# Performance work log

Hardware: AMD Instinct MI355X
Metric: run time of the kernel (lower is better)

Reference implementation:

```python
import jax, jax.numpy as jnp
import numpy as np

B, S, D = 4, 2048, 1024
H, DK, DV = 16, 64, 64
SCALE = 8.0  # scaling_factor = sqrt(dk)


def setup_inputs() -> dict:
    key = jax.random.key(0)
    ks = jax.random.split(key, 9)
    s = 1.0 / np.sqrt(D)
    return {
        "q": jax.random.normal(ks[0], (B, S, D), jnp.float32),
        "k": jax.random.normal(ks[1], (B, S, D), jnp.float32),
        "v": jax.random.normal(ks[2], (B, S, D), jnp.float32),
        "Wq": jax.random.uniform(ks[3], (D, H * DK), jnp.float32, -s, s),
        "bq": jax.random.uniform(ks[4], (H * DK,), jnp.float32, -s, s),
        "Wk": jax.random.uniform(ks[5], (D, H * DK), jnp.float32, -s, s),
        "bk": jax.random.uniform(ks[6], (H * DK,), jnp.float32, -s, s),
        "Wv": jax.random.uniform(ks[7], (D, H * DV), jnp.float32, -s, s),
        "bv": jax.random.uniform(ks[8], (H * DV,), jnp.float32, -s, s),
    }


def reference(q, k, v, Wq, bq, Wk, bk, Wv, bv):
    # Linear projections, then split heads: [B,S,H*d] -> [B,S,H,d]
    qh = (q @ Wq + bq).reshape(B, S, H, DK)
    kh = (k @ Wk + bk).reshape(B, S, H, DK)
    vh = (v @ Wv + bv).reshape(B, S, H, DV)
    # scores: [B,H,Sq,Sk]
    e = jnp.einsum("bqhd,bkhd->bhqk", qh, kh) / SCALE
    attn = jax.nn.softmax(e, axis=-1)
    out = jnp.einsum("bhqk,bkhd->bqhd", attn, vh)  # [B,Sq,H,DV]
    return out.reshape(B, S, H * DV)  # dropout p=0 -> identity
```

## Files before the change

### kernel.cpp

```cpp
#include <hip/hip_runtime.h>
#include <hip/hip_bf16.h>


typedef unsigned short u16;
typedef unsigned int   u32;
typedef short bf16x8 __attribute__((ext_vector_type(8)));
typedef short bf16x4 __attribute__((ext_vector_type(4)));
typedef float f32x4  __attribute__((ext_vector_type(4)));
typedef u32   u32x4  __attribute__((ext_vector_type(4)));

#define S_TOT 2048
#define HD    1024
#define QK_SCALE 0.18033688f

#if __has_builtin(__builtin_amdgcn_exp2f)
#define EXP2(x) __builtin_amdgcn_exp2f(x)
#else
#define EXP2(x) exp2f(x)
#endif

__device__ __forceinline__ u16 f2bf(float f) {
  union { float f; unsigned u; } v; v.f = f;
  unsigned r = v.u + 0x7FFFu + ((v.u >> 16) & 1u);
  return (u16)(r >> 16);
}

__device__ __forceinline__ u32 cvt_pk_bf16(float lo, float hi) {
  u32 r;
  asm("v_cvt_pk_bf16_f32 %0, %1, %2" : "=v"(r) : "v"(lo), "v"(hi));
  return r;
}

__device__ __forceinline__ bf16x4 ds_tr16(unsigned a) {
  bf16x4 d;
  asm volatile("ds_read_b64_tr_b16 %0, %1" : "=v"(d) : "v"(a) : "memory");
  return d;
}

__device__ __forceinline__ void gld16(const u16* g, u16* l) {
  __builtin_amdgcn_global_load_lds(
      (const __attribute__((address_space(1))) u32*)g,
      (__attribute__((address_space(3))) u32*)l, 16, 0, 0);
}

#define LGKM_FENCE() do { asm volatile("s_waitcnt lgkmcnt(0)" ::: "memory"); \
                          __builtin_amdgcn_sched_barrier(0); } while (0)

__global__ __launch_bounds__(256)
void conv_kernel(const float* __restrict__ x0, const float* __restrict__ x1, const float* __restrict__ x2,
                 const float* __restrict__ w0, const float* __restrict__ w1, const float* __restrict__ w2,
                 u16* __restrict__ Xb, u16* __restrict__ Wt)
{
  const int z = blockIdx.y;
  const int t = threadIdx.x;
  if (blockIdx.x < 1024) {
    const float* X = z == 0 ? x0 : (z == 1 ? x1 : x2);
    u16* Xz = Xb + (size_t)z * 8388608;
    int tid = blockIdx.x * 256 + t;
#pragma unroll
    for (int i = 0; i < 8; ++i) {
      int c = tid + i * 262144;
      int row = c >> 8, k4 = (c & 255) * 4;
      const float4 xv = *(const float4*)&X[(size_t)row * 1024 + k4];
      int p = (k4 & ~31) + 8 * ((k4 & 15) >> 2) + 4 * ((k4 >> 4) & 1);
      bf16x4 sv = { (short)f2bf(xv.x), (short)f2bf(xv.y), (short)f2bf(xv.z), (short)f2bf(xv.w) };
      *(bf16x4*)&Xz[(size_t)row * 1024 + p] = sv;
    }
  } else {
    const float* W = z == 0 ? w0 : (z == 1 ? w1 : w2);
    u16* Wz = Wt + (size_t)z * 1048576;
    int tid = (blockIdx.x - 1024) * 256 + t;
#pragma unroll
    for (int i = 0; i < 8; ++i) {
      int c = tid + i * 32768;
      int k = c >> 8, n4 = (c & 255) * 4;
      const float4 wv = *(const float4*)&W[(size_t)k * 1024 + n4];
      int off = ((n4 >> 7) * 32 + (k >> 5)) * 4096 + ((n4 >> 4) & 7) * 512
              + ((k >> 4) & 1) * 256 + (k & 15) * 16 + (n4 & 15);
      bf16x4 sv = { (short)f2bf(wv.x), (short)f2bf(wv.y), (short)f2bf(wv.z), (short)f2bf(wv.w) };
      *(bf16x4*)&Wz[off] = sv;
    }
  }
}

__global__ __launch_bounds__(256)
void gemm_kernel(const u16* __restrict__ Xb, const u16* __restrict__ Wt,
                 const float* __restrict__ b0, const float* __restrict__ b1, const float* __restrict__ b2,
                 u16* __restrict__ o0, u16* __restrict__ o1, u16* __restrict__ o2)
{
  int p  = blockIdx.x + 8 * blockIdx.y + 512 * blockIdx.z;
  int wk = (p & 7) * 192 + (p >> 3);
  int nb = wk & 7, mb = (wk >> 3) & 63, z = wk >> 9;

  const u16* Xz = Xb + (size_t)z * 8388608;
  const u16* Wz = Wt + (size_t)z * 1048576;
  const float* BS = z == 0 ? b0 : (z == 1 ? b1 : b2);
  u16*         O  = z == 0 ? o0 : (z == 1 ? o1 : o2);
  const float  osc = (z == 0) ? QK_SCALE : 1.0f;

  const int t = threadIdx.x;
  const int lane = t & 63, wid = t >> 6;
  const int g = lane >> 4, ln = lane & 15;
  const int wm = wid >> 1, wn = wid & 1;
  const int mbase = mb * 128, nbase = nb * 128;

  __shared__ __align__(16) u16 Al[128 * 32];
  __shared__ __align__(16) u16 Bl[16 * 256];

  f32x4 acc[4][4];
#pragma unroll
  for (int i = 0; i < 4; ++i)
#pragma unroll
    for (int j = 0; j < 4; ++j) { acc[i][j][0]=0.f; acc[i][j][1]=0.f; acc[i][j][2]=0.f; acc[i][j][3]=0.f; }

  const u16* sa = Xz + (size_t)(mbase + (t >> 2)) * 1024 + (t & 3) * 8;
  const u16* sb = Wz + (size_t)(nb * 32) * 4096 + t * 8;
  u16* al_w = &Al[wid * 512];
  u16* bl_w = &Bl[wid * 512];

  const unsigned bs_base = (unsigned)(size_t)&Bl[0] + (unsigned)((wn * 4) * 1024) + lane * 8;

  for (int kb = 0; kb < 32; ++kb) {
    gld16(sa + kb * 32,                 al_w);
    gld16(sa + kb * 32 + 64 * 1024,     al_w + 2048);
    gld16(sb + kb * 4096,               bl_w);
    gld16(sb + kb * 4096 + 2048,        bl_w + 2048);
    __syncthreads();

    bf16x8 af[4];
#pragma unroll
    for (int mf = 0; mf < 4; ++mf)
      af[mf] = *(const bf16x8*)&Al[(wm * 64 + mf * 16 + ln) * 32 + g * 8];

    bf16x8 bfv[4];
#pragma unroll
    for (int nf = 0; nf < 4; ++nf) {
      bf16x4 lo = ds_tr16(bs_base + (unsigned)(nf * 1024));
      bf16x4 hi = ds_tr16(bs_base + (unsigned)(nf * 1024 + 512));
      bf16x8 bb;
      bb[0]=lo[0]; bb[1]=lo[1]; bb[2]=lo[2]; bb[3]=lo[3];
      bb[4]=hi[0]; bb[5]=hi[1]; bb[6]=hi[2]; bb[7]=hi[3];
      bfv[nf] = bb;
    }
    LGKM_FENCE();
#pragma unroll
    for (int mf = 0; mf < 4; ++mf)
#pragma unroll
      for (int nf = 0; nf < 4; ++nf)
        acc[mf][nf] = __builtin_amdgcn_mfma_f32_16x16x32_bf16(af[mf], bfv[nf], acc[mf][nf], 0, 0, 0);
    __syncthreads();
  }

#pragma unroll
  for (int nf = 0; nf < 4; ++nf) {
    int n = nbase + wn * 64 + nf * 16 + ln;
    float bv = BS[n];
#pragma unroll
    for (int mf = 0; mf < 4; ++mf)
#pragma unroll
      for (int r = 0; r < 4; ++r) {
        int m = mbase + wm * 64 + mf * 16 + 4 * g + r;
        O[(size_t)m * 1024 + n] = f2bf((acc[mf][nf][r] + bv) * osc);
      }
  }
}

__global__ __launch_bounds__(256)
void proj_kernel(const float* __restrict__ x0, const float* __restrict__ x1, const float* __restrict__ x2,
                 const float* __restrict__ w0, const float* __restrict__ w1, const float* __restrict__ w2,
                 const float* __restrict__ b0, const float* __restrict__ b1, const float* __restrict__ b2,
                 u16* __restrict__ o0, u16* __restrict__ o1, u16* __restrict__ o2)
{
  int p  = blockIdx.x + 8 * blockIdx.y + 512 * blockIdx.z;
  int wk = (p & 7) * 192 + (p >> 3);
  int nb = wk & 7, mb = (wk >> 3) & 63, z = wk >> 9;

  const float* X  = z == 0 ? x0 : (z == 1 ? x1 : x2);
  const float* W  = z == 0 ? w0 : (z == 1 ? w1 : w2);
  const float* BS = z == 0 ? b0 : (z == 1 ? b1 : b2);
  u16*         O  = z == 0 ? o0 : (z == 1 ? o1 : o2);
  const float  osc = (z == 0) ? QK_SCALE : 1.0f;

  const int t = threadIdx.x;
  const int lane = t & 63, wid = t >> 6;
  const int g = lane >> 4, ln = lane & 15;
  const int wm = wid >> 1, wn = wid & 1;
  const int mbase = mb * 128, nbase = nb * 128;

  __shared__ __align__(16) u16 As[128 * 40];
  __shared__ __align__(16) u16 Bs[16 * 272];

  f32x4 acc[4][4];
#pragma unroll
  for (int i = 0; i < 4; ++i)
#pragma unroll
    for (int j = 0; j < 4; ++j) { acc[i][j][0]=0.f; acc[i][j][1]=0.f; acc[i][j][2]=0.f; acc[i][j][3]=0.f; }

  const int arow = t >> 3;
  const int ak0  = (t & 7) * 4;
  const int ap   = 8 * ((ak0 & 15) >> 2) + 4 * (ak0 >> 4);
  const int bkr  = t >> 5;
  const int bnc  = (t & 31) * 4;
  const int bnblk = bnc >> 4, bncl = bnc & 15;

  const unsigned bs_base = (unsigned)(size_t)&Bs[0];

  for (int kb = 0; kb < 32; ++kb) {
    const int kbase = kb * 32;
#pragma unroll
    for (int ps = 0; ps < 4; ++ps) {
      int row = arow + 32 * ps;
      const float4 xv = *(const float4*)&X[(size_t)(mbase + row) * 1024 + kbase + ak0];
      bf16x4 sv = { (short)f2bf(xv.x), (short)f2bf(xv.y), (short)f2bf(xv.z), (short)f2bf(xv.w) };
      *(bf16x4*)&As[row * 40 + ap] = sv;
    }
#pragma unroll
    for (int ps = 0; ps < 4; ++ps) {
      int kr = bkr + 8 * ps;
      const float4 wv = *(const float4*)&W[(size_t)(kbase + kr) * 1024 + nbase + bnc];
      bf16x4 sv = { (short)f2bf(wv.x), (short)f2bf(wv.y), (short)f2bf(wv.z), (short)f2bf(wv.w) };
      *(bf16x4*)&Bs[(bnblk * 2 + (kr >> 4)) * 272 + (kr & 15) * 16 + bncl] = sv;
    }
    __syncthreads();

    bf16x8 af[4];
#pragma unroll
    for (int mf = 0; mf < 4; ++mf)
      af[mf] = *(const bf16x8*)&As[(wm * 64 + mf * 16 + ln) * 40 + g * 8];

    bf16x8 bfv[4];
#pragma unroll
    for (int nf = 0; nf < 4; ++nf) {
      unsigned base = bs_base + (unsigned)(((wn * 4 + nf) * 2) * 544) + lane * 8;
      bf16x4 lo = ds_tr16(base);
      bf16x4 hi = ds_tr16(base + 544);
      bf16x8 bb;
      bb[0]=lo[0]; bb[1]=lo[1]; bb[2]=lo[2]; bb[3]=lo[3];
      bb[4]=hi[0]; bb[5]=hi[1]; bb[6]=hi[2]; bb[7]=hi[3];
      bfv[nf] = bb;
    }
    LGKM_FENCE();
#pragma unroll
    for (int mf = 0; mf < 4; ++mf)
#pragma unroll
      for (int nf = 0; nf < 4; ++nf)
        acc[mf][nf] = __builtin_amdgcn_mfma_f32_16x16x32_bf16(af[mf], bfv[nf], acc[mf][nf], 0, 0, 0);
    __syncthreads();
  }

#pragma unroll
  for (int nf = 0; nf < 4; ++nf) {
    int n = nbase + wn * 64 + nf * 16 + ln;
    float bv = BS[n];
#pragma unroll
    for (int mf = 0; mf < 4; ++mf)
#pragma unroll
      for (int r = 0; r < 4; ++r) {
        int m = mbase + wm * 64 + mf * 16 + 4 * g + r;
        O[(size_t)m * 1024 + n] = f2bf((acc[mf][nf][r] + bv) * osc);
      }
  }
}

__global__ __launch_bounds__(512)
void attn_kernel(const u16* __restrict__ qh, const u16* __restrict__ kh, const u16* __restrict__ vh,
                 float* __restrict__ out)
{
  int p  = blockIdx.x + 8 * blockIdx.y + 128 * blockIdx.z;
  int wk = (p & 7) * 64 + (p >> 3);
  int qt = wk & 7, h = (wk >> 3) & 15, b = wk >> 7;

  const int t = threadIdx.x;
  const int lane = t & 63, wid = t >> 6;
  const int g = lane >> 4, ln = lane & 15;
  const size_t bS = (size_t)b * S_TOT;
  const int qwin = qt * 256 + wid * 32;

  __shared__ __align__(16) u16 Ks[64 * 72];
  __shared__ __align__(16) u16 Vs[16 * 272];

  bf16x8 qf[2][2];
#pragma unroll
  for (int nf = 0; nf < 2; ++nf) {
    const u16* qrow = &qh[(bS + qwin + nf * 16 + ln) * HD + h * 64];
#pragma unroll
    for (int kk = 0; kk < 2; ++kk) {
      bf16x4 lo = *(const bf16x4*)&qrow[kk * 32 + 4 * g];
      bf16x4 hi = *(const bf16x4*)&qrow[kk * 32 + 4 * g + 16];
      bf16x8 qq;
      qq[0]=lo[0]; qq[1]=lo[1]; qq[2]=lo[2]; qq[3]=lo[3];
      qq[4]=hi[0]; qq[5]=hi[1]; qq[6]=hi[2]; qq[7]=hi[3];
      qf[nf][kk] = qq;
    }
  }

  bf16x8 ones;
#pragma unroll
  for (int j = 0; j < 8; ++j) ones[j] = (short)0x3F80;

  f32x4 o[2][4];
#pragma unroll
  for (int i = 0; i < 2; ++i)
#pragma unroll
    for (int j = 0; j < 4; ++j) { o[i][j][0]=0.f; o[i][j][1]=0.f; o[i][j][2]=0.f; o[i][j][3]=0.f; }
  f32x4 o1[2];
  o1[0][0]=0.f; o1[0][1]=0.f; o1[0][2]=0.f; o1[0][3]=0.f;
  o1[1][0]=0.f; o1[1][1]=0.f; o1[1][2]=0.f; o1[1][3]=0.f;

  const unsigned vs_base = (unsigned)(size_t)&Vs[0] + lane * 8;
  const int skv = t >> 4;
  const int sd0 = (t & 15) * 4;
  const int kpos = 32 * (sd0 >> 5) + 8 * ((sd0 & 15) >> 2) + 4 * ((sd0 >> 4) & 1);

  u16* ksw[2]; u16* vsw[2];
#pragma unroll
  for (int c = 0; c < 2; ++c) {
    ksw[c] = &Ks[(skv + 32 * c) * 72 + kpos];
    vsw[c] = &Vs[((sd0 >> 4) * 4 + (skv >> 4) + 2 * c) * 272 + (skv & 15) * 16 + (sd0 & 15)];
  }
  const u16* kp = &kh[(bS + skv) * HD + h * 64 + sd0];
  const u16* vp = &vh[(bS + skv) * HD + h * 64 + sd0];
  const size_t STEP64 = (size_t)64 * HD, C32 = (size_t)32 * HD;

  bf16x4 kr[2], vr[2];
#pragma unroll
  for (int c = 0; c < 2; ++c) {
    kr[c] = *(const bf16x4*)(kp + c * C32);
    vr[c] = *(const bf16x4*)(vp + c * C32);
  }
  kp += STEP64; vp += STEP64;

  for (int it = 0; it < 32; ++it) {
#pragma unroll
    for (int c = 0; c < 2; ++c) { *(bf16x4*)ksw[c] = kr[c]; *(bf16x4*)vsw[c] = vr[c]; }
    __syncthreads();

    if (it < 31) {
#pragma unroll
      for (int c = 0; c < 2; ++c) {
        kr[c] = *(const bf16x4*)(kp + c * C32);
        vr[c] = *(const bf16x4*)(vp + c * C32);
      }
      kp += STEP64; vp += STEP64;
    }

#pragma unroll
    for (int s = 0; s < 2; ++s) {
      bf16x8 kf[2][2];
#pragma unroll
      for (int mf = 0; mf < 2; ++mf)
#pragma unroll
        for (int kk = 0; kk < 2; ++kk)
          kf[mf][kk] = *(const bf16x8*)&Ks[(s * 32 + mf * 16 + ln) * 72 + kk * 32 + 8 * g];

      f32x4 sc[2][2];
      __builtin_amdgcn_s_setprio(1);
#pragma unroll
      for (int mf = 0; mf < 2; ++mf)
#pragma unroll
        for (int nf = 0; nf < 2; ++nf) {
          f32x4 a; a[0]=0.f; a[1]=0.f; a[2]=0.f; a[3]=0.f;
#pragma unroll
          for (int kk = 0; kk < 2; ++kk)
            a = __builtin_amdgcn_mfma_f32_16x16x32_bf16(kf[mf][kk], qf[nf][kk], a, 0, 0, 0);
          sc[mf][nf] = a;
        }
      __builtin_amdgcn_s_setprio(0);

      bf16x8 vf[4];
#pragma unroll
      for (int nf = 0; nf < 4; ++nf) {
        bf16x4 lo = ds_tr16(vs_base + (unsigned)((nf * 4 + 2 * s) * 544));
        bf16x4 hi = ds_tr16(vs_base + (unsigned)((nf * 4 + 2 * s + 1) * 544));
        bf16x8 bb;
        bb[0]=lo[0]; bb[1]=lo[1]; bb[2]=lo[2]; bb[3]=lo[3];
        bb[4]=hi[0]; bb[5]=hi[1]; bb[6]=hi[2]; bb[7]=hi[3];
        vf[nf] = bb;
      }

      bf16x8 pa[2];
#pragma unroll
      for (int nf = 0; nf < 2; ++nf) {
        float pv[2][4];
#pragma unroll
        for (int mf = 0; mf < 2; ++mf)
#pragma unroll
          for (int r = 0; r < 4; ++r)
            pv[mf][r] = EXP2(sc[mf][nf][r]);
        union { u32x4 u; bf16x8 b; } pk;
        pk.u[0] = cvt_pk_bf16(pv[0][0], pv[0][1]);
        pk.u[1] = cvt_pk_bf16(pv[0][2], pv[0][3]);
        pk.u[2] = cvt_pk_bf16(pv[1][0], pv[1][1]);
        pk.u[3] = cvt_pk_bf16(pv[1][2], pv[1][3]);
        pa[nf] = pk.b;
      }

      LGKM_FENCE();
      __builtin_amdgcn_s_setprio(1);
#pragma unroll
      for (int mq = 0; mq < 2; ++mq) {
#pragma unroll
        for (int nf = 0; nf < 4; ++nf)
          o[mq][nf] = __builtin_amdgcn_mfma_f32_16x16x32_bf16(pa[mq], vf[nf], o[mq][nf], 0, 0, 0);
        o1[mq] = __builtin_amdgcn_mfma_f32_16x16x32_bf16(pa[mq], ones, o1[mq], 0, 0, 0);
      }
      __builtin_amdgcn_s_setprio(0);
    }
    __syncthreads();
  }

#pragma unroll
  for (int mq = 0; mq < 2; ++mq)
#pragma unroll
    for (int r = 0; r < 4; ++r) {
      float inv = 1.0f / o1[mq][r];
      int qrow = qwin + mq * 16 + 4 * g + r;
#pragma unroll
      for (int nf = 0; nf < 4; ++nf)
        out[(bS + qrow) * HD + h * 64 + nf * 16 + ln] = o[mq][nf][r] * inv;
    }
}

extern "C" void kernel_launch(void* const* d_in, const int* in_sizes, int n_in,
                              void* d_out, int out_size, void* d_ws, size_t ws_size,
                              hipStream_t stream) {
  const float* q  = (const float*)d_in[0];
  const float* k  = (const float*)d_in[1];
  const float* v  = (const float*)d_in[2];
  const float* Wq = (const float*)d_in[3];
  const float* bq = (const float*)d_in[4];
  const float* Wk = (const float*)d_in[5];
  const float* bk = (const float*)d_in[6];
  const float* Wv = (const float*)d_in[7];
  const float* bv = (const float*)d_in[8];
  float* out = (float*)d_out;

  u16* qh = (u16*)d_ws;
  u16* kh = qh + (size_t)8192 * 1024;
  u16* vh = kh + (size_t)8192 * 1024;

  const size_t XB_OFF = (size_t)3 * 8192 * 1024;
  const size_t WT_OFF = XB_OFF + (size_t)3 * 8192 * 1024;
  const size_t NEED   = (WT_OFF + (size_t)3 * 1024 * 1024) * 2;

  if (ws_size >= NEED) {
    u16* Xb = (u16*)d_ws + XB_OFF;
    u16* Wt = (u16*)d_ws + WT_OFF;
    conv_kernel<<<dim3(1152, 3), 256, 0, stream>>>(q, k, v, Wq, Wk, Wv, Xb, Wt);
    gemm_kernel<<<dim3(8, 64, 3), 256, 0, stream>>>(Xb, Wt, bq, bk, bv, qh, kh, vh);
  } else {
    proj_kernel<<<dim3(8, 64, 3), 256, 0, stream>>>(q, k, v, Wq, Wk, Wv, bq, bk, bv, qh, kh, vh);
  }
  attn_kernel<<<dim3(8, 16, 4), 512, 0, stream>>>(qh, kh, vh, out);
}
```

Measured before the change: 186.8 us.

## Write V projection transposed per head so attention loads V without LDS transpose

The V projection GEMM now computes the transposed product (W^T X^T) and writes V in a [B,H,DV,S] layout. The attention kernel can then stage V tiles with plain row loads into padded LDS and read its MFMA operands with ordinary vector loads instead of ds_read transpose instructions. The aim is cheaper V staging and operand fetch inside the attention loop. The cost is a strided, scattered 2-byte global store pattern in the V projection epilogue, which may hurt that GEMM.

```diff
diff --git a/kernel.cpp b/kernel.cpp
--- a/kernel.cpp
+++ b/kernel.cpp
@@ -86,7 +86,7 @@
 __global__ __launch_bounds__(256)
 void gemm_kernel(const u16* __restrict__ Xb, const u16* __restrict__ Wt,
                  const float* __restrict__ b0, const float* __restrict__ b1, const float* __restrict__ b2,
-                 u16* __restrict__ o0, u16* __restrict__ o1, u16* __restrict__ o2)
+                 u16* __restrict__ o0, u16* __restrict__ o1, u16* __restrict__ vT)
 {
   int p  = blockIdx.x + 8 * blockIdx.y + 512 * blockIdx.z;
   int wk = (p & 7) * 192 + (p >> 3);
@@ -95,13 +95,11 @@
   const u16* Xz = Xb + (size_t)z * 8388608;
   const u16* Wz = Wt + (size_t)z * 1048576;
   const float* BS = z == 0 ? b0 : (z == 1 ? b1 : b2);
-  u16*         O  = z == 0 ? o0 : (z == 1 ? o1 : o2);
   const float  osc = (z == 0) ? QK_SCALE : 1.0f;
 
   const int t = threadIdx.x;
   const int lane = t & 63, wid = t >> 6;
   const int g = lane >> 4, ln = lane & 15;
-  const int wm = wid >> 1, wn = wid & 1;
   const int mbase = mb * 128, nbase = nb * 128;
 
   __shared__ __align__(16) u16 Al[128 * 32];
@@ -118,49 +116,101 @@
   u16* al_w = &Al[wid * 512];
   u16* bl_w = &Bl[wid * 512];
 
-  const unsigned bs_base = (unsigned)(size_t)&Bl[0] + (unsigned)((wn * 4) * 1024) + lane * 8;
-
-  for (int kb = 0; kb < 32; ++kb) {
-    gld16(sa + kb * 32,                 al_w);
-    gld16(sa + kb * 32 + 64 * 1024,     al_w + 2048);
-    gld16(sb + kb * 4096,               bl_w);
-    gld16(sb + kb * 4096 + 2048,        bl_w + 2048);
-    __syncthreads();
-
-    bf16x8 af[4];
+  if (z < 2) {
+    const int wm = wid >> 1, wn = wid & 1;
+    u16* O = z == 0 ? o0 : o1;
+    const unsigned bs_base = (unsigned)(size_t)&Bl[0] + (unsigned)((wn * 4) * 1024) + lane * 8;
+
+    for (int kb = 0; kb < 32; ++kb) {
+      gld16(sa + kb * 32,                 al_w);
+      gld16(sa + kb * 32 + 64 * 1024,     al_w + 2048);
+      gld16(sb + kb * 4096,               bl_w);
+      gld16(sb + kb * 4096 + 2048,        bl_w + 2048);
+      __syncthreads();
+
+      bf16x8 af[4];
+#pragma unroll
+      for (int mf = 0; mf < 4; ++mf)
+        af[mf] = *(const bf16x8*)&Al[(wm * 64 + mf * 16 + ln) * 32 + g * 8];
+
+      bf16x8 bfv[4];
+#pragma unroll
+      for (int nf = 0; nf < 4; ++nf) {
+        bf16x4 lo = ds_tr16(bs_base + (unsigned)(nf * 1024));
+        bf16x4 hi = ds_tr16(bs_base + (unsigned)(nf * 1024 + 512));
+        bf16x8 bb;
+        bb[0]=lo[0]; bb[1]=lo[1]; bb[2]=lo[2]; bb[3]=lo[3];
+        bb[4]=hi[0]; bb[5]=hi[1]; bb[6]=hi[2]; bb[7]=hi[3];
+        bfv[nf] = bb;
+      }
+      LGKM_FENCE();
+#pragma unroll
+      for (int mf = 0; mf < 4; ++mf)
+#pragma unroll
+        for (int nf = 0; nf < 4; ++nf)
+          acc[mf][nf] = __builtin_amdgcn_mfma_f32_16x16x32_bf16(af[mf], bfv[nf], acc[mf][nf], 0, 0, 0);
+      __syncthreads();
+    }
+
+#pragma unroll
+    for (int nf = 0; nf < 4; ++nf) {
+      int n = nbase + wn * 64 + nf * 16 + ln;
+      float bv = BS[n];
+#pragma unroll
+      for (int mf = 0; mf < 4; ++mf)
+#pragma unroll
+        for (int r = 0; r < 4; ++r) {
+          int m = mbase + wm * 64 + mf * 16 + 4 * g + r;
+          O[(size_t)m * 1024 + n] = f2bf((acc[mf][nf][r] + bv) * osc);
+        }
+    }
+  } else {
+    const int wseq = wid >> 1, wdv = wid & 1;
+    const unsigned bs_base2 = (unsigned)(size_t)&Bl[0] + (unsigned)((wdv * 4) * 1024) + lane * 8;
+
+    for (int kb = 0; kb < 32; ++kb) {
+      gld16(sa + kb * 32,                 al_w);
+      gld16(sa + kb * 32 + 64 * 1024,     al_w + 2048);
+      gld16(sb + kb * 4096,               bl_w);
+      gld16(sb + kb * 4096 + 2048,        bl_w + 2048);
+      __syncthreads();
+
+      bf16x8 afw[4];
+#pragma unroll
+      for (int mf = 0; mf < 4; ++mf) {
+        bf16x4 lo = ds_tr16(bs_base2 + (unsigned)(mf * 1024));
+        bf16x4 hi = ds_tr16(bs_base2 + (unsigned)(mf * 1024 + 512));
+        bf16x8 bb;
+        bb[0]=lo[0]; bb[1]=lo[1]; bb[2]=lo[2]; bb[3]=lo[3];
+        bb[4]=hi[0]; bb[5]=hi[1]; bb[6]=hi[2]; bb[7]=hi[3];
+        afw[mf] = bb;
+      }
+      bf16x8 bfx[4];
+#pragma unroll
+      for (int nf = 0; nf < 4; ++nf)
+        bfx[nf] = *(const bf16x8*)&Al[(wseq * 64 + nf * 16 + ln) * 32 + g * 8];
+      LGKM_FENCE();
+#pragma unroll
+      for (int mf = 0; mf < 4; ++mf)
+#pragma unroll
+        for (int nf = 0; nf < 4; ++nf)
+          acc[mf][nf] = __builtin_amdgcn_mfma_f32_16x16x32_bf16(afw[mf], bfx[nf], acc[mf][nf], 0, 0, 0);
+      __syncthreads();
+    }
+
 #pragma unroll
     for (int mf = 0; mf < 4; ++mf)
-      af[mf] = *(const bf16x8*)&Al[(wm * 64 + mf * 16 + ln) * 32 + g * 8];
-
-    bf16x8 bfv[4];
-#pragma unroll
-    for (int nf = 0; nf < 4; ++nf) {
-      bf16x4 lo = ds_tr16(bs_base + (unsigned)(nf * 1024));
-      bf16x4 hi = ds_tr16(bs_base + (unsigned)(nf * 1024 + 512));
-      bf16x8 bb;
-      bb[0]=lo[0]; bb[1]=lo[1]; bb[2]=lo[2]; bb[3]=lo[3];
-      bb[4]=hi[0]; bb[5]=hi[1]; bb[6]=hi[2]; bb[7]=hi[3];
-      bfv[nf] = bb;
-    }
-    LGKM_FENCE();
-#pragma unroll
-    for (int mf = 0; mf < 4; ++mf)
-#pragma unroll
-      for (int nf = 0; nf < 4; ++nf)
-        acc[mf][nf] = __builtin_amdgcn_mfma_f32_16x16x32_bf16(af[mf], bfv[nf], acc[mf][nf], 0, 0, 0);
-    __syncthreads();
-  }
-
-#pragma unroll
-  for (int nf = 0; nf < 4; ++nf) {
-    int n = nbase + wn * 64 + nf * 16 + ln;
-    float bv = BS[n];
-#pragma unroll
-    for (int mf = 0; mf < 4; ++mf)
 #pragma unroll
       for (int r = 0; r < 4; ++r) {
-        int m = mbase + wm * 64 + mf * 16 + 4 * g + r;
-        O[(size_t)m * 1024 + n] = f2bf((acc[mf][nf][r] + bv) * osc);
+        int dvg = nbase + wdv * 64 + mf * 16 + 4 * g + r;
+        float bv = BS[dvg];
+        int hh = dvg >> 6, dvl = dvg & 63;
+#pragma unroll
+        for (int nf = 0; nf < 4; ++nf) {
+          int m = mbase + wseq * 64 + nf * 16 + ln;
+          int bb = m >> 11, ss = m & 2047;
+          vT[((size_t)(bb * 16 + hh) * 64 + dvl) * 2048 + ss] = f2bf(acc[mf][nf][r] + bv);
+        }
       }
   }
 }
@@ -169,7 +219,7 @@
 void proj_kernel(const float* __restrict__ x0, const float* __restrict__ x1, const float* __restrict__ x2,
                  const float* __restrict__ w0, const float* __restrict__ w1, const float* __restrict__ w2,
                  const float* __restrict__ b0, const float* __restrict__ b1, const float* __restrict__ b2,
-                 u16* __restrict__ o0, u16* __restrict__ o1, u16* __restrict__ o2)
+                 u16* __restrict__ o0, u16* __restrict__ o1, u16* __restrict__ vT)
 {
   int p  = blockIdx.x + 8 * blockIdx.y + 512 * blockIdx.z;
   int wk = (p & 7) * 192 + (p >> 3);
@@ -178,7 +228,6 @@
   const float* X  = z == 0 ? x0 : (z == 1 ? x1 : x2);
   const float* W  = z == 0 ? w0 : (z == 1 ? w1 : w2);
   const float* BS = z == 0 ? b0 : (z == 1 ? b1 : b2);
-  u16*         O  = z == 0 ? o0 : (z == 1 ? o1 : o2);
   const float  osc = (z == 0) ? QK_SCALE : 1.0f;
 
   const int t = threadIdx.x;
@@ -257,13 +306,19 @@
 #pragma unroll
       for (int r = 0; r < 4; ++r) {
         int m = mbase + wm * 64 + mf * 16 + 4 * g + r;
-        O[(size_t)m * 1024 + n] = f2bf((acc[mf][nf][r] + bv) * osc);
+        float val = (acc[mf][nf][r] + bv) * osc;
+        if (z < 2) {
+          u16* O = z == 0 ? o0 : o1;
+          O[(size_t)m * 1024 + n] = f2bf(val);
+        } else {
+          vT[((size_t)((m >> 11) * 16 + (n >> 6)) * 64 + (n & 63)) * 2048 + (m & 2047)] = f2bf(val);
+        }
       }
   }
 }
 
 __global__ __launch_bounds__(512)
-void attn_kernel(const u16* __restrict__ qh, const u16* __restrict__ kh, const u16* __restrict__ vh,
+void attn_kernel(const u16* __restrict__ qh, const u16* __restrict__ kh, const u16* __restrict__ vT,
                  float* __restrict__ out)
 {
   int p  = blockIdx.x + 8 * blockIdx.y + 128 * blockIdx.z;
@@ -277,7 +332,7 @@
   const int qwin = qt * 256 + wid * 32;
 
   __shared__ __align__(16) u16 Ks[64 * 72];
-  __shared__ __align__(16) u16 Vs[16 * 272];
+  __shared__ __align__(16) u16 Vt[64 * 72];
 
   bf16x8 qf[2][2];
 #pragma unroll
@@ -307,41 +362,43 @@
   o1[0][0]=0.f; o1[0][1]=0.f; o1[0][2]=0.f; o1[0][3]=0.f;
   o1[1][0]=0.f; o1[1][1]=0.f; o1[1][2]=0.f; o1[1][3]=0.f;
 
-  const unsigned vs_base = (unsigned)(size_t)&Vs[0] + lane * 8;
   const int skv = t >> 4;
   const int sd0 = (t & 15) * 4;
   const int kpos = 32 * (sd0 >> 5) + 8 * ((sd0 & 15) >> 2) + 4 * ((sd0 >> 4) & 1);
-
-  u16* ksw[2]; u16* vsw[2];
-#pragma unroll
-  for (int c = 0; c < 2; ++c) {
-    ksw[c] = &Ks[(skv + 32 * c) * 72 + kpos];
-    vsw[c] = &Vs[((sd0 >> 4) * 4 + (skv >> 4) + 2 * c) * 272 + (skv & 15) * 16 + (sd0 & 15)];
-  }
+  u16* ksw[2];
+  ksw[0] = &Ks[skv * 72 + kpos];
+  ksw[1] = &Ks[(skv + 32) * 72 + kpos];
   const u16* kp = &kh[(bS + skv) * HD + h * 64 + sd0];
-  const u16* vp = &vh[(bS + skv) * HD + h * 64 + sd0];
-  const size_t STEP64 = (size_t)64 * HD, C32 = (size_t)32 * HD;
-
-  bf16x4 kr[2], vr[2];
-#pragma unroll
-  for (int c = 0; c < 2; ++c) {
-    kr[c] = *(const bf16x4*)(kp + c * C32);
-    vr[c] = *(const bf16x4*)(vp + c * C32);
-  }
-  kp += STEP64; vp += STEP64;
+
+  const int vdv  = t >> 3;
+  const int vkv8 = (t & 7) * 8;
+  const int vp0  = 32 * (vkv8 >> 5) + 8 * ((vkv8 & 15) >> 2) + 4 * ((vkv8 >> 4) & 1);
+  const int vkv4 = vkv8 + 4;
+  const int vp1  = 32 * (vkv4 >> 5) + 8 * ((vkv4 & 15) >> 2) + 4 * ((vkv4 >> 4) & 1);
+  u16* vsw0 = &Vt[vdv * 72 + vp0];
+  u16* vsw1 = &Vt[vdv * 72 + vp1];
+  const u16* vp = &vT[((size_t)(b * 16 + h) * 64 + vdv) * 2048 + vkv8];
+
+  const size_t KSTEP = (size_t)64 * HD, C32 = (size_t)32 * HD;
+
+  bf16x4 kr[2];
+  kr[0] = *(const bf16x4*)kp; kr[1] = *(const bf16x4*)(kp + C32);
+  bf16x8 vr = *(const bf16x8*)vp;
+  kp += KSTEP; vp += 64;
 
   for (int it = 0; it < 32; ++it) {
-#pragma unroll
-    for (int c = 0; c < 2; ++c) { *(bf16x4*)ksw[c] = kr[c]; *(bf16x4*)vsw[c] = vr[c]; }
+    *(bf16x4*)ksw[0] = kr[0];
+    *(bf16x4*)ksw[1] = kr[1];
+    bf16x4 vlo = { vr[0], vr[1], vr[2], vr[3] };
+    bf16x4 vhi = { vr[4], vr[5], vr[6], vr[7] };
+    *(bf16x4*)vsw0 = vlo;
+    *(bf16x4*)vsw1 = vhi;
     __syncthreads();
 
     if (it < 31) {
-#pragma unroll
-      for (int c = 0; c < 2; ++c) {
-        kr[c] = *(const bf16x4*)(kp + c * C32);
-        vr[c] = *(const bf16x4*)(vp + c * C32);
-      }
-      kp += STEP64; vp += STEP64;
+      kr[0] = *(const bf16x4*)kp; kr[1] = *(const bf16x4*)(kp + C32);
+      vr = *(const bf16x8*)vp;
+      kp += KSTEP; vp += 64;
     }
 
 #pragma unroll
@@ -369,14 +426,8 @@
 
       bf16x8 vf[4];
 #pragma unroll
-      for (int nf = 0; nf < 4; ++nf) {
-        bf16x4 lo = ds_tr16(vs_base + (unsigned)((nf * 4 + 2 * s) * 544));
-        bf16x4 hi = ds_tr16(vs_base + (unsigned)((nf * 4 + 2 * s + 1) * 544));
-        bf16x8 bb;
-        bb[0]=lo[0]; bb[1]=lo[1]; bb[2]=lo[2]; bb[3]=lo[3];
-        bb[4]=hi[0]; bb[5]=hi[1]; bb[6]=hi[2]; bb[7]=hi[3];
-        vf[nf] = bb;
-      }
+      for (int nf = 0; nf < 4; ++nf)
+        vf[nf] = *(const bf16x8*)&Vt[(nf * 16 + ln) * 72 + s * 32 + 8 * g];
 
       bf16x8 pa[2];
 #pragma unroll
@@ -395,7 +446,6 @@
         pa[nf] = pk.b;
       }
 
-      LGKM_FENCE();
       __builtin_amdgcn_s_setprio(1);
 #pragma unroll
       for (int mq = 0; mq < 2; ++mq) {
@@ -437,7 +487,7 @@
 
   u16* qh = (u16*)d_ws;
   u16* kh = qh + (size_t)8192 * 1024;
-  u16* vh = kh + (size_t)8192 * 1024;
+  u16* vT = kh + (size_t)8192 * 1024;
 
   const size_t XB_OFF = (size_t)3 * 8192 * 1024;
   const size_t WT_OFF = XB_OFF + (size_t)3 * 8192 * 1024;
@@ -447,9 +497,9 @@
     u16* Xb = (u16*)d_ws + XB_OFF;
     u16* Wt = (u16*)d_ws + WT_OFF;
     conv_kernel<<<dim3(1152, 3), 256, 0, stream>>>(q, k, v, Wq, Wk, Wv, Xb, Wt);
-    gemm_kernel<<<dim3(8, 64, 3), 256, 0, stream>>>(Xb, Wt, bq, bk, bv, qh, kh, vh);
+    gemm_kernel<<<dim3(8, 64, 3), 256, 0, stream>>>(Xb, Wt, bq, bk, bv, qh, kh, vT);
   } else {
-    proj_kernel<<<dim3(8, 64, 3), 256, 0, stream>>>(q, k, v, Wq, Wk, Wv, bq, bk, bv, qh, kh, vh);
-  }
-  attn_kernel<<<dim3(8, 16, 4), 512, 0, stream>>>(qh, kh, vh, out);
-}
+    proj_kernel<<<dim3(8, 64, 3), 256, 0, stream>>>(q, k, v, Wq, Wk, Wv, bq, bk, bv, qh, kh, vT);
+  }
+  attn_kernel<<<dim3(8, 16, 4), 512, 0, stream>>>(qh, kh, vT, out);
+}
```

After: 178.6 us. 4.4% less time.
